# Performance work log

Measured on AMD Instinct MI355X. Metric: run time of the kernel, lower is better.

## Reference

```python
import jax, jax.numpy as jnp
import numpy as np

N, H, E, H1, H2, S = 64, 128, 32, 128, 64, 4096
U, I, L = 32, 32, 16
D = U + I + L + S + 2 * S  # linear input dim = num_features + 2*num_skills
P = H * (H - 1) // 2
# strictly-lower-triangular pair indices, row-major (i, j<i) -- matches the torch mask order
I_IDX, J_IDX = np.tril_indices(H, -1)
I_IDX = jnp.asarray(I_IDX)
J_IDX = jnp.asarray(J_IDX)


def setup_inputs() -> dict:
    key = jax.random.key(0)
    ks = jax.random.split(key, 16)
    skills = jax.random.randint(ks[0], (N, H), 1, S)  # avoid padding idx 0 for realism
    targets = jax.random.bernoulli(ks[1], 0.5, (N, H)).astype(jnp.float32)
    users = jax.random.normal(ks[2], (N, U), jnp.float32)
    items = jax.random.normal(ks[3], (N * H, I), jnp.float32)
    langs = jax.random.normal(ks[4], (N * H, L), jnp.float32)
    mask = jax.random.bernoulli(ks[5], 0.8, (N * H,))
    emb_table = (0.02 * jax.random.normal(ks[6], (S, E), jnp.float32)).at[0].set(0.0)  # padding_idx=0
    W1 = 0.05 * jax.random.normal(ks[7], (2 * E, H1), jnp.float32)
    b1 = jnp.zeros((H1,), jnp.float32)
    W2 = 0.05 * jax.random.normal(ks[8], (H1, H2), jnp.float32)
    b2 = jnp.zeros((H2,), jnp.float32)
    Ws = 0.05 * jax.random.normal(ks[9], (H2, 1), jnp.float32)
    bs = jnp.zeros((1,), jnp.float32)
    Wlin = 0.01 * jax.random.normal(ks[10], (D, 1), jnp.float32)
    blin = jnp.zeros((1,), jnp.float32)
    return dict(skills=skills, targets=targets, users=users, items=items, langs=langs,
                mask=mask, emb_table=emb_table, W1=W1, b1=b1, W2=W2, b2=b2,
                Ws=Ws, bs=bs, Wlin=Wlin, blin=blin)


def reference(skills, targets, users, items, langs, mask,
              emb_table, W1, b1, W2, b2, Ws, bs, Wlin, blin):
    # ---- compute_correct_total ----
    emb = emb_table[skills]                      # [N, H, E] gather
    e_i = emb[:, I_IDX]                          # current skill emb per pair [N, P, E]
    e_j = emb[:, J_IDX]                          # history skill emb per pair [N, P, E]
    x = jnp.concatenate([e_i, e_j], axis=-1)     # [N, P, 2E]
    h = jax.nn.relu(x @ W1 + b1)                 # dropout = 0 (eval)
    h = jax.nn.relu(h @ W2 + b2)
    sim = jnp.tanh(h @ Ws + bs)[..., 0]          # [N, P]
    # per-position segment sums: seg[n, i] = sum_{j<i} sim[n, (i,j)]
    seg_total = jnp.zeros((N, H), jnp.float32).at[:, I_IDX].add(sim)
    sim_correct = sim * targets[:, J_IDX]        # weight by history correctness
    seg_correct = jnp.zeros((N, H), jnp.float32).at[:, I_IDX].add(sim_correct)
    # per-skill scatter-add into dense [N, 2S] feature tensor
    rows = jnp.arange(N)[:, None]
    tcf = (jnp.zeros((N, 2 * S), jnp.float32)
           .at[rows, skills].add(seg_total)
           .at[rows, skills + S].add(seg_correct))
    # ---- forward ----
    onehot = jax.nn.one_hot(skills.reshape(-1), S, dtype=jnp.float32)   # [N*H, S]
    feats = jnp.concatenate([
        jnp.repeat(users, H, axis=0),            # repeat_interleave over seq positions
        items, langs, onehot,
        jnp.repeat(tcf, H, axis=0),
    ], axis=1)                                   # [N*H, D]
    logits = feats @ Wlin + blin                 # [N*H, 1]
    z = logits.reshape(-1)
    y = targets.reshape(-1)
    m = mask.astype(jnp.float32)
    # masked mean BCE-with-logits (z_weight = 0)
    bce = jnp.maximum(z, 0.0) - z * y + jnp.log1p(jnp.exp(-jnp.abs(z)))
    loss = jnp.sum(bce * m) / jnp.maximum(jnp.sum(m), 1.0)
    return loss, jax.nn.sigmoid(logits)
```

## Files before the change

kernel.cpp:

```cpp
#include <hip/hip_runtime.h>
#include <hip/hip_fp16.h>

#define N_ 64
#define H_ 128
#define E_ 32
#define H1_ 128
#define H2_ 64
#define S_ 4096
#define OFF_ITEMS 32
#define OFF_LANGS 64
#define OFF_ONEHOT 80
#define OFF_TCF 4176
#define OFF_TCF2 8272

typedef _Float16 half8 __attribute__((ext_vector_type(8)));
typedef short short8 __attribute__((ext_vector_type(8)));
typedef float floatx4 __attribute__((ext_vector_type(4)));

__global__ void build_w2frag(const float* __restrict__ W2, _Float16* __restrict__ W2f) {
    int f = blockIdx.x * 256 + threadIdx.x;
    int e  = f & 7;
    int lo = (f >> 3) & 15;
    int hi = (f >> 7) & 3;
    int nt = (f >> 9) & 3;
    int kk = f >> 11;
    W2f[f] = (_Float16)W2[(32 * kk + 8 * hi + e) * 64 + (16 * nt + lo)];
}

__global__ void build_ab(const int* __restrict__ skills,
                         const float* __restrict__ emb_table,
                         const float* __restrict__ W1,
                         const float* __restrict__ b1,
                         _Float16* __restrict__ aT, _Float16* __restrict__ bT) {
    __shared__ float W1s[64 * 128];
    __shared__ float embs[16][32];

    int tid = threadIdx.x;
    for (int idx = tid; idx < 64 * 128; idx += 256) W1s[idx] = W1[idx];

    int r0 = blockIdx.x * 16;
    for (int idx = tid; idx < 16 * 32; idx += 256) {
        int r = idx >> 5, e = idx & 31;
        int sk = skills[r0 + r];
        embs[r][e] = emb_table[sk * 32 + e];
    }
    __syncthreads();

    int k = tid & 127;
    int rh = tid >> 7;
    float b1k = b1[k];
    for (int rr = 0; rr < 16; rr += 2) {
        int r = rr + rh;
        float a = b1k, b = 0.f;
        #pragma unroll
        for (int e = 0; e < 32; e++) {
            float ev = embs[r][e];
            a += ev * W1s[e * 128 + k];
            b += ev * W1s[(e + 32) * 128 + k];
        }
        size_t row = (size_t)(r0 + r) * 128;
        aT[row + k] = (_Float16)a;
        bT[row + k] = (_Float16)b;
    }
}

__global__ __launch_bounds__(256) void pair_mlp(
    const _Float16* __restrict__ aT, const _Float16* __restrict__ bT,
    const _Float16* __restrict__ W2f, const float* __restrict__ targets,
    const float* __restrict__ b2, const float* __restrict__ Ws,
    const float* __restrict__ bs,
    float* __restrict__ segT, float* __restrict__ segC) {

    int bid = blockIdx.x;
    int n = bid / 10;
    int t = bid % 10;
    int ti = 0;
    while ((ti + 1) * (ti + 2) / 2 <= t) ti++;
    int tj = t - ti * (ti + 1) / 2;
    int i0 = ti * 32, j0 = tj * 32;
    bool diag = (ti == tj);

    __shared__ __align__(16) _Float16 aL[32][136];
    __shared__ __align__(16) _Float16 bL[32][136];
    __shared__ float tgt[32];

    int tid = threadIdx.x;
    for (int idx = tid; idx < 512; idx += 256) {
        int r = idx >> 4, c = idx & 15;
        *(uint4*)(&aL[r][c * 8]) = *(const uint4*)(aT + (size_t)(n * H_ + i0 + r) * 128 + c * 8);
        *(uint4*)(&bL[r][c * 8]) = *(const uint4*)(bT + (size_t)(n * H_ + j0 + r) * 128 + c * 8);
    }
    if (tid < 32) tgt[tid] = targets[n * H_ + j0 + tid];

    int lane = tid & 63, wv = tid >> 6;
    int hi = lane >> 4, lo = lane & 15;

    half8 wfrag[4][4];
    #pragma unroll
    for (int kk = 0; kk < 4; kk++)
        #pragma unroll
        for (int nt = 0; nt < 4; nt++)
            wfrag[kk][nt] = *(const half8*)(W2f + ((((kk * 4 + nt) * 4 + hi) * 16 + lo) * 8));

    float b2v[4], wsv[4];
    #pragma unroll
    for (int nt = 0; nt < 4; nt++) {
        b2v[nt] = b2[16 * nt + lo];
        wsv[nt] = Ws[16 * nt + lo];
    }
    float bsv = bs[0];

    __syncthreads();

    for (int g = wv; g < 64; g += 4) {
        int li = g >> 1;
        int hf = g & 1;
        if (diag && li <= 16 * hf) continue;

        const _Float16* arow = &aL[li][0];
        const _Float16* brow = &bL[16 * hf + lo][0];

        floatx4 acc[4];
        #pragma unroll
        for (int nt = 0; nt < 4; nt++) acc[nt] = (floatx4){0.f, 0.f, 0.f, 0.f};

        #pragma unroll
        for (int kk = 0; kk < 4; kk++) {
            half8 av = *(const half8*)(arow + 32 * kk + 8 * hi);
            half8 bv = *(const half8*)(brow + 32 * kk + 8 * hi);
            half8 s = av + bv;
            short8 bits = __builtin_bit_cast(short8, s);
            short8 sgn = bits >> 15;
            bits &= ~sgn;
            half8 h = __builtin_bit_cast(half8, bits);
            acc[0] = __builtin_amdgcn_mfma_f32_16x16x32_f16(h, wfrag[kk][0], acc[0], 0, 0, 0);
            acc[1] = __builtin_amdgcn_mfma_f32_16x16x32_f16(h, wfrag[kk][1], acc[1], 0, 0, 0);
            acc[2] = __builtin_amdgcn_mfma_f32_16x16x32_f16(h, wfrag[kk][2], acc[2], 0, 0, 0);
            acc[3] = __builtin_amdgcn_mfma_f32_16x16x32_f16(h, wfrag[kk][3], acc[3], 0, 0, 0);
        }

        float part[4];
        #pragma unroll
        for (int r4 = 0; r4 < 4; r4++) {
            float p = 0.f;
            #pragma unroll
            for (int nt = 0; nt < 4; nt++)
                p += fmaxf(acc[nt][r4] + b2v[nt], 0.f) * wsv[nt];
            part[r4] = p;
        }
        #pragma unroll
        for (int m = 1; m <= 8; m <<= 1) {
            #pragma unroll
            for (int r4 = 0; r4 < 4; r4++)
                part[r4] += __shfl_xor(part[r4], m, 64);
        }
        float sumT = 0.f, sumC = 0.f;
        #pragma unroll
        for (int r4 = 0; r4 < 4; r4++) {
            int srow = 4 * hi + r4;
            int lj = 16 * hf + srow;
            bool valid = (!diag) || (li > lj);
            float x = part[r4] + bsv;
            float e2 = __expf(2.f * x);
            float sv = (e2 - 1.f) / (e2 + 1.f);
            sv = valid ? sv : 0.f;
            sumT += sv;
            sumC += sv * tgt[lj];
        }
        sumT += __shfl_xor(sumT, 16, 64);
        sumT += __shfl_xor(sumT, 32, 64);
        sumC += __shfl_xor(sumC, 16, 64);
        sumC += __shfl_xor(sumC, 32, 64);
        if (lane == 0) {
            atomicAdd(&segT[n * H_ + i0 + li], sumT);
            atomicAdd(&segC[n * H_ + i0 + li], sumC);
        }
    }
}

__global__ void finalize(const int* __restrict__ skills,
                         const float* __restrict__ targets,
                         const float* __restrict__ users,
                         const float* __restrict__ items,
                         const float* __restrict__ langs,
                         const void* __restrict__ mask,
                         const float* __restrict__ Wlin,
                         const float* __restrict__ blin,
                         const float* __restrict__ segT,
                         const float* __restrict__ segC,
                         float* __restrict__ out,
                         float* __restrict__ accums) {
    int n = blockIdx.x, h = threadIdx.x;
    int nh = n * H_ + h;
    int sk = skills[nh];

    const unsigned* mw = (const unsigned*)mask;
    bool byte_layout = false;
    #pragma unroll 8
    for (int q = 0; q < 64; q++) byte_layout |= (mw[q] > 1u);
    float m = byte_layout ? (((const unsigned char*)mask)[nh] ? 1.f : 0.f)
                          : (mw[nh] ? 1.f : 0.f);

    float tterm = segT[nh] * Wlin[OFF_TCF + sk] + segC[nh] * Wlin[OFF_TCF2 + sk];
    if (h < 32) tterm += users[n * 32 + h] * Wlin[h];

    __shared__ float red[128];
    red[h] = tterm;
    __syncthreads();
    for (int s = 64; s > 0; s >>= 1) {
        if (h < s) red[h] += red[h + s];
        __syncthreads();
    }
    float c = red[0] + blin[0];
    __syncthreads();

    float z = c + Wlin[OFF_ONEHOT + sk];
    #pragma unroll
    for (int i = 0; i < 32; i++) z += items[(size_t)nh * 32 + i] * Wlin[OFF_ITEMS + i];
    #pragma unroll
    for (int l = 0; l < 16; l++) z += langs[(size_t)nh * 16 + l] * Wlin[OFF_LANGS + l];

    out[1 + nh] = 1.f / (1.f + __expf(-z));

    float y = targets[nh];
    float bce = fmaxf(z, 0.f) - z * y + log1pf(__expf(-fabsf(z)));

    red[h] = bce * m;
    __syncthreads();
    for (int s = 64; s > 0; s >>= 1) {
        if (h < s) red[h] += red[h + s];
        __syncthreads();
    }
    if (h == 0) atomicAdd(&accums[0], red[0]);
    __syncthreads();

    red[h] = m;
    __syncthreads();
    for (int s = 64; s > 0; s >>= 1) {
        if (h < s) red[h] += red[h + s];
        __syncthreads();
    }
    if (h == 0) atomicAdd(&accums[1], red[0]);
}

__global__ void finalize_loss(const float* __restrict__ accums, float* __restrict__ out) {
    out[0] = accums[0] / fmaxf(accums[1], 1.f);
}

extern "C" void kernel_launch(void* const* d_in, const int* in_sizes, int n_in,
                              void* d_out, int out_size, void* d_ws, size_t ws_size,
                              hipStream_t stream) {
    const int*   skills  = (const int*)d_in[0];
    const float* targets = (const float*)d_in[1];
    const float* users   = (const float*)d_in[2];
    const float* items   = (const float*)d_in[3];
    const float* langs   = (const float*)d_in[4];
    const void*  mask    = (const void*)d_in[5];
    const float* emb     = (const float*)d_in[6];
    const float* W1      = (const float*)d_in[7];
    const float* b1      = (const float*)d_in[8];
    const float* W2      = (const float*)d_in[9];
    const float* b2      = (const float*)d_in[10];
    const float* Ws      = (const float*)d_in[11];
    const float* bs      = (const float*)d_in[12];
    const float* Wlin    = (const float*)d_in[13];
    const float* blin    = (const float*)d_in[14];

    char* ws = (char*)d_ws;
    _Float16* aT  = (_Float16*)(ws);
    _Float16* bT  = (_Float16*)(ws + (2u << 20));
    _Float16* W2f = (_Float16*)(ws + (4u << 20));
    float* segT   = (float*)(ws + (4u << 20) + 16384);
    float* segC   = segT + N_ * H_;
    float* accums = segC + N_ * H_;

    hipMemsetAsync(segT, 0, (size_t)(2 * N_ * H_ + 2) * sizeof(float), stream);

    build_w2frag<<<32, 256, 0, stream>>>(W2, W2f);
    build_ab<<<512, 256, 0, stream>>>(skills, emb, W1, b1, aT, bT);
    pair_mlp<<<N_ * 10, 256, 0, stream>>>(aT, bT, W2f, targets, b2, Ws, bs, segT, segC);
    finalize<<<N_, H_, 0, stream>>>(skills, targets, users, items, langs, mask,
                                    Wlin, blin, segT, segC, (float*)d_out, accums);
    finalize_loss<<<1, 1, 0, stream>>>(accums, (float*)d_out);
}
```

Before: 135.5 us.

## Merge prep kernels and memset, fold loss into finalize, reduce atomics

Merges the W2 fragment build, the zeroing of the accumulators and the A/B build into a single prep launch, with one extra block handling the zeroing and W2 conversion. The final loss kernel is removed by having the last finalize block compute the loss behind an atomic counter. In pair_mlp, per-row sums are accumulated in shared memory first, so each block issues only one set of global atomics. Finalize also uses float4 loads and a combined reduction, and the mask-layout probe is shortened from 64 to 16 words, which is a small risk if the probe misses the layout. The goal is fewer launches and less atomic traffic.

```diff
diff --git a/kernel.cpp b/kernel.cpp
--- a/kernel.cpp
+++ b/kernel.cpp
@@ -17,25 +17,32 @@
 typedef short short8 __attribute__((ext_vector_type(8)));
 typedef float floatx4 __attribute__((ext_vector_type(4)));
 
-__global__ void build_w2frag(const float* __restrict__ W2, _Float16* __restrict__ W2f) {
-    int f = blockIdx.x * 256 + threadIdx.x;
-    int e  = f & 7;
-    int lo = (f >> 3) & 15;
-    int hi = (f >> 7) & 3;
-    int nt = (f >> 9) & 3;
-    int kk = f >> 11;
-    W2f[f] = (_Float16)W2[(32 * kk + 8 * hi + e) * 64 + (16 * nt + lo)];
-}
-
-__global__ void build_ab(const int* __restrict__ skills,
-                         const float* __restrict__ emb_table,
-                         const float* __restrict__ W1,
-                         const float* __restrict__ b1,
-                         _Float16* __restrict__ aT, _Float16* __restrict__ bT) {
+__global__ __launch_bounds__(256) void prep(
+    const int* __restrict__ skills, const float* __restrict__ emb_table,
+    const float* __restrict__ W1, const float* __restrict__ b1,
+    const float* __restrict__ W2,
+    _Float16* __restrict__ aT, _Float16* __restrict__ bT,
+    _Float16* __restrict__ W2f, float* __restrict__ zero_region) {
+
+    int tid = threadIdx.x;
+
+    if (blockIdx.x == 512) {
+        for (int idx = tid; idx < 2 * N_ * H_ + 4; idx += 256)
+            zero_region[idx] = 0.f;
+        for (int f = tid; f < 8192; f += 256) {
+            int e  = f & 7;
+            int lo = (f >> 3) & 15;
+            int hi = (f >> 7) & 3;
+            int nt = (f >> 9) & 3;
+            int kk = f >> 11;
+            W2f[f] = (_Float16)W2[(32 * kk + 8 * hi + e) * 64 + (16 * nt + lo)];
+        }
+        return;
+    }
+
     __shared__ float W1s[64 * 128];
     __shared__ float embs[16][32];
 
-    int tid = threadIdx.x;
     for (int idx = tid; idx < 64 * 128; idx += 256) W1s[idx] = W1[idx];
 
     int r0 = blockIdx.x * 16;
@@ -83,6 +90,7 @@
     __shared__ __align__(16) _Float16 aL[32][136];
     __shared__ __align__(16) _Float16 bL[32][136];
     __shared__ float tgt[32];
+    __shared__ float sT[32], sC[32];
 
     int tid = threadIdx.x;
     for (int idx = tid; idx < 512; idx += 256) {
@@ -90,7 +98,11 @@
         *(uint4*)(&aL[r][c * 8]) = *(const uint4*)(aT + (size_t)(n * H_ + i0 + r) * 128 + c * 8);
         *(uint4*)(&bL[r][c * 8]) = *(const uint4*)(bT + (size_t)(n * H_ + j0 + r) * 128 + c * 8);
     }
-    if (tid < 32) tgt[tid] = targets[n * H_ + j0 + tid];
+    if (tid < 32) {
+        tgt[tid] = targets[n * H_ + j0 + tid];
+        sT[tid] = 0.f;
+        sC[tid] = 0.f;
+    }
 
     int lane = tid & 63, wv = tid >> 6;
     int hi = lane >> 4, lo = lane & 15;
@@ -167,14 +179,16 @@
             sumT += sv;
             sumC += sv * tgt[lj];
         }
-        sumT += __shfl_xor(sumT, 16, 64);
-        sumT += __shfl_xor(sumT, 32, 64);
-        sumC += __shfl_xor(sumC, 16, 64);
-        sumC += __shfl_xor(sumC, 32, 64);
-        if (lane == 0) {
-            atomicAdd(&segT[n * H_ + i0 + li], sumT);
-            atomicAdd(&segC[n * H_ + i0 + li], sumC);
-        }
+        if (lo == 0) {
+            atomicAdd(&sT[li], sumT);
+            atomicAdd(&sC[li], sumC);
+        }
+    }
+
+    __syncthreads();
+    if (tid < 32) {
+        atomicAdd(&segT[n * H_ + i0 + tid], sT[tid]);
+        atomicAdd(&segC[n * H_ + i0 + tid], sC[tid]);
     }
 }
 
@@ -189,15 +203,16 @@
                          const float* __restrict__ segT,
                          const float* __restrict__ segC,
                          float* __restrict__ out,
-                         float* __restrict__ accums) {
+                         float* __restrict__ accums,
+                         int* __restrict__ counter) {
     int n = blockIdx.x, h = threadIdx.x;
     int nh = n * H_ + h;
     int sk = skills[nh];
 
     const unsigned* mw = (const unsigned*)mask;
     bool byte_layout = false;
-    #pragma unroll 8
-    for (int q = 0; q < 64; q++) byte_layout |= (mw[q] > 1u);
+    #pragma unroll
+    for (int q = 0; q < 16; q++) byte_layout |= (mw[q] > 1u);
     float m = byte_layout ? (((const unsigned char*)mask)[nh] ? 1.f : 0.f)
                           : (mw[nh] ? 1.f : 0.f);
 
@@ -212,39 +227,48 @@
         __syncthreads();
     }
     float c = red[0] + blin[0];
-    __syncthreads();
 
     float z = c + Wlin[OFF_ONEHOT + sk];
-    #pragma unroll
-    for (int i = 0; i < 32; i++) z += items[(size_t)nh * 32 + i] * Wlin[OFF_ITEMS + i];
-    #pragma unroll
-    for (int l = 0; l < 16; l++) z += langs[(size_t)nh * 16 + l] * Wlin[OFF_LANGS + l];
+    const float4* ip = (const float4*)(items + (size_t)nh * 32);
+    #pragma unroll
+    for (int i4 = 0; i4 < 8; i4++) {
+        float4 v = ip[i4];
+        z += v.x * Wlin[OFF_ITEMS + 4 * i4]     + v.y * Wlin[OFF_ITEMS + 4 * i4 + 1]
+           + v.z * Wlin[OFF_ITEMS + 4 * i4 + 2] + v.w * Wlin[OFF_ITEMS + 4 * i4 + 3];
+    }
+    const float4* lp = (const float4*)(langs + (size_t)nh * 16);
+    #pragma unroll
+    for (int l4 = 0; l4 < 4; l4++) {
+        float4 v = lp[l4];
+        z += v.x * Wlin[OFF_LANGS + 4 * l4]     + v.y * Wlin[OFF_LANGS + 4 * l4 + 1]
+           + v.z * Wlin[OFF_LANGS + 4 * l4 + 2] + v.w * Wlin[OFF_LANGS + 4 * l4 + 3];
+    }
 
     out[1 + nh] = 1.f / (1.f + __expf(-z));
 
     float y = targets[nh];
     float bce = fmaxf(z, 0.f) - z * y + log1pf(__expf(-fabsf(z)));
 
-    red[h] = bce * m;
+    __shared__ float2 red2[128];
+    red2[h] = make_float2(bce * m, m);
     __syncthreads();
     for (int s = 64; s > 0; s >>= 1) {
-        if (h < s) red[h] += red[h + s];
+        if (h < s) {
+            red2[h].x += red2[h + s].x;
+            red2[h].y += red2[h + s].y;
+        }
         __syncthreads();
     }
-    if (h == 0) atomicAdd(&accums[0], red[0]);
-    __syncthreads();
-
-    red[h] = m;
-    __syncthreads();
-    for (int s = 64; s > 0; s >>= 1) {
-        if (h < s) red[h] += red[h + s];
-        __syncthreads();
-    }
-    if (h == 0) atomicAdd(&accums[1], red[0]);
-}
-
-__global__ void finalize_loss(const float* __restrict__ accums, float* __restrict__ out) {
-    out[0] = accums[0] / fmaxf(accums[1], 1.f);
+    if (h == 0) {
+        atomicAdd(&accums[0], red2[0].x);
+        atomicAdd(&accums[1], red2[0].y);
+        __threadfence();
+        if (atomicAdd(counter, 1) == N_ - 1) {
+            float a = atomicAdd(&accums[0], 0.f);
+            float b = atomicAdd(&accums[1], 0.f);
+            out[0] = a / fmaxf(b, 1.f);
+        }
+    }
 }
 
 extern "C" void kernel_launch(void* const* d_in, const int* in_sizes, int n_in,
@@ -273,13 +297,10 @@
     float* segT   = (float*)(ws + (4u << 20) + 16384);
     float* segC   = segT + N_ * H_;
     float* accums = segC + N_ * H_;
-
-    hipMemsetAsync(segT, 0, (size_t)(2 * N_ * H_ + 2) * sizeof(float), stream);
-
-    build_w2frag<<<32, 256, 0, stream>>>(W2, W2f);
-    build_ab<<<512, 256, 0, stream>>>(skills, emb, W1, b1, aT, bT);
+    int*   counter = (int*)(accums + 2);
+
+    prep<<<513, 256, 0, stream>>>(skills, emb, W1, b1, W2, aT, bT, W2f, segT);
     pair_mlp<<<N_ * 10, 256, 0, stream>>>(aT, bT, W2f, targets, b2, Ws, bs, segT, segC);
     finalize<<<N_, H_, 0, stream>>>(skills, targets, users, items, langs, mask,
-                                    Wlin, blin, segT, segC, (float*)d_out, accums);
-    finalize_loss<<<1, 1, 0, stream>>>(accums, (float*)d_out);
+                                    Wlin, blin, segT, segC, (float*)d_out, accums, counter);
 }
```

New measurement: 134.4 us. No clear change (-0.8%).
